# Performance work log

Measured on AMD Instinct MI355X. Metric: run time of the kernel, lower is better.

Reference implementation:

```python
import jax, jax.numpy as jnp
import numpy as np

WEIGHT = 1.0  # configer affinity_loss weight


def setup_inputs() -> dict:
    key = jax.random.key(0)
    k1, k2, k3, k4, k5 = jax.random.split(key, 5)
    bz, C, h, w = 4, 21, 32, 32
    token_n = h * w            # 1024
    total_n = token_n + 1      # 1025 (CLS token in encoder attns)
    head_n = 8
    return {
        "preds": jax.random.normal(k1, (bz, C, h, w), dtype=jnp.float32),
        "low_feats": jnp.zeros((1,), dtype=jnp.float32),
        "high_feats": jnp.zeros((1,), dtype=jnp.float32),
        "unlabeled_ROIs": jax.random.randint(k2, (bz, h, w), 0, 2, dtype=jnp.int32),
        "targets": jax.random.randint(k3, (bz, h, w), 0, C),
        # raw (pre-renormalization) positive attention maps, stacked over 2 layers
        "attns": jax.random.uniform(k4, (2, bz, head_n, total_n, total_n), dtype=jnp.float32),
        "decode_attns": jax.random.uniform(k5, (2, bz, head_n, token_n, token_n), dtype=jnp.float32),
    }


def reference(preds, low_feats, high_feats, unlabeled_ROIs, targets, attns, decode_attns):
    # loss_index=2, gt_add=0
    bz, C, h, w = preds.shape
    token_n = h * w
    Le = attns.shape[0]
    Ld = decode_attns.shape[0]

    # Encoder attentions: drop CLS row/col, row-normalize, average over heads & layers.
    enc = attns[:, :, :, 1:, 1:]                         # (Le, b, H, t, t)
    enc = enc / enc.sum(axis=-1, keepdims=True)
    encode_attn_avg = enc.mean(axis=(0, 2))              # (b, t, t)

    # Decoder attentions: crop to token_n, row-normalize, average over heads & layers.
    dec = decode_attns[:, :, :, :token_n, :token_n]
    dec = dec / dec.sum(axis=-1, keepdims=True)
    decode_attn_avg = dec.mean(axis=(0, 2))              # (b, t, t)

    total_attn_avg = (encode_attn_avg * Le + decode_attn_avg * Ld) / (Le + Ld)

    # Class probabilities per token: (b, t, C)
    prob = jax.nn.softmax(preds, axis=1).reshape(bz, C, token_n).transpose(0, 2, 1)

    # The broadcast-multiply-sum over dim=2 is exactly a batched matmul.
    affinity_prob = jnp.einsum('bij,bjc->bic', total_attn_avg, prob)
    affinity_prob = affinity_prob / affinity_prob.sum(axis=-1, keepdims=True)

    # nearest-interp to (h, w) is the identity here (ROIs already at (h, w))
    roi = unlabeled_ROIs.astype(jnp.float32).reshape(bz, token_n, 1)
    N = roi.sum()
    loss = (roi * jnp.abs(prob - affinity_prob)).sum()
    loss = jnp.where(N > 0, loss / N, loss)
    return WEIGHT * loss
```

## Files before the change

### kernel.cpp

```cpp
#include <hip/hip_runtime.h>
#include <cstdint>
#include <cstddef>

#define C_N     21
#define BZ      4
#define TOKEN_N 1024
#define TOTAL_N 1025
#define PROB_ELEMS (BZ * TOKEN_N * C_N)
#define ENC_TOT  67240000ull

typedef short  short8 __attribute__((ext_vector_type(8)));
typedef float  f32x4  __attribute__((ext_vector_type(4)));

typedef __attribute__((address_space(1))) const unsigned int* gld_gp;
typedef __attribute__((address_space(3))) unsigned int*       gld_lp;

static __device__ __forceinline__ unsigned int f2bf(float x) {
    unsigned int u = __float_as_uint(x);
    return (u + 0x7FFFu + ((u >> 16) & 1u)) >> 16;
}

__global__ __launch_bounds__(256) void softmax_kernel(const float* __restrict__ preds,
                                                      float* __restrict__ prob) {
    int t = blockIdx.x * blockDim.x + threadIdx.x;
    if (t >= BZ * TOKEN_N) return;
    int b = t >> 10, j = t & 1023;
    const float* p = preds + (size_t)b * C_N * TOKEN_N + j;
    float v[C_N];
    float mx = -3.4e38f;
#pragma unroll
    for (int c = 0; c < C_N; ++c) { v[c] = p[(size_t)c * TOKEN_N]; mx = fmaxf(mx, v[c]); }
    float ss = 0.f;
#pragma unroll
    for (int c = 0; c < C_N; ++c) { v[c] = __expf(v[c] - mx); ss += v[c]; }
    float inv = 1.f / ss;
    float* o = prob + (size_t)t * C_N;
#pragma unroll
    for (int c = 0; c < C_N; ++c) o[c] = v[c] * inv;
}

__global__ __launch_bounds__(256) void bpack2_kernel(const float* __restrict__ prob,
                                                     uint4* __restrict__ bp) {
    int idx = blockIdx.x * 256 + threadIdx.x;
    if (idx >= BZ * 32 * 2 * 64) return;
    int lane = idx & 63;
    int nt   = (idx >> 6) & 1;
    int kk   = (idx >> 7) & 31;
    int b    = idx >> 12;
    int n    = (lane & 15) + nt * 16;
    int k0   = kk * 32 + ((lane >> 4) << 3);
    unsigned int h[8];
#pragma unroll
    for (int e = 0; e < 8; ++e) {
        float v;
        if (n < C_N)       v = prob[((size_t)b * TOKEN_N + (k0 + e)) * C_N + n];
        else if (n == C_N) v = 1.0f;
        else               v = 0.0f;
        h[e] = f2bf(v);
    }
    uint4 o;
    o.x = h[0] | (h[1] << 16);
    o.y = h[2] | (h[3] << 16);
    o.z = h[4] | (h[5] << 16);
    o.w = h[6] | (h[7] << 16);
    bp[idx] = o;
}

template<bool ENC>
__device__ __forceinline__ void rows_body(const float* __restrict__ base, int mm, int i0,
                                          const uint4* __restrict__ bp,
                                          float* __restrict__ acc, float* __restrict__ lds) {
    const int tid  = threadIdx.x;
    const int lane = tid & 63;
    const int w    = tid >> 6;
    const int b    = (mm >> 3) & 3;

    int delta = 0;
    if constexpr (ENC) {
        const size_t S0 = (size_t)mm * 1050625ull + (size_t)(1 + i0) * 1025ull + 1ull;
        const size_t aligned = S0 & ~(size_t)3;
        delta = (int)(S0 - aligned);
        const int nInstr = (w < 3) ? 17 : 14;
        const int e0 = w * 17;
        for (int q = 0; q < nInstr; ++q) {
            const int e = e0 + q;
            size_t gb  = aligned + (size_t)e * 256;
            int   ldso = e * 256;
            if (gb + 256 > ENC_TOT) {
                size_t d = gb + 256 - ENC_TOT;
                gb -= d; ldso -= (int)d;
            }
            __builtin_amdgcn_global_load_lds((gld_gp)(base + gb + (size_t)lane * 4),
                                             (gld_lp)&lds[ldso], 16, 0, 0);
        }
    } else {
        const size_t sb = (size_t)mm * 1048576ull + (size_t)i0 * 1024ull;
#pragma unroll
        for (int q = 0; q < 16; ++q) {
            const int e = w * 16 + q;
            const int row = e >> 2, sub = e & 3;
            const size_t gb = sb + (size_t)row * 1024 + (size_t)sub * 256;
            const int ldso  = row * 1028 + sub * 256;
            __builtin_amdgcn_global_load_lds((gld_gp)(base + gb + (size_t)lane * 4),
                                             (gld_lp)&lds[ldso], 16, 0, 0);
        }
    }

    const uint4* bpp = bp + (size_t)b * 4096 + lane;
    uint4 Bq[8][2];
#pragma unroll
    for (int s = 0; s < 8; ++s) {
        Bq[s][0] = bpp[(w * 8 + s) * 128];
        Bq[s][1] = bpp[(w * 8 + s) * 128 + 64];
    }

    __syncthreads();

    const int r = lane & 15, kg = lane >> 4;
    f32x4 c0 = {0.f, 0.f, 0.f, 0.f};
    f32x4 c1 = {0.f, 0.f, 0.f, 0.f};
#pragma unroll
    for (int s = 0; s < 8; ++s) {
        const int k0 = w * 256 + s * 32 + kg * 8;
        float a0, a1, a2, a3, a4, a5, a6, a7;
        if constexpr (ENC) {
            const float* p = lds + delta + r * 1025 + k0;
            a0 = p[0]; a1 = p[1]; a2 = p[2]; a3 = p[3];
            a4 = p[4]; a5 = p[5]; a6 = p[6]; a7 = p[7];
        } else {
            const float* p = lds + r * 1028 + k0;
            float4 lo = *reinterpret_cast<const float4*>(p);
            float4 hi = *reinterpret_cast<const float4*>(p + 4);
            a0 = lo.x; a1 = lo.y; a2 = lo.z; a3 = lo.w;
            a4 = hi.x; a5 = hi.y; a6 = hi.z; a7 = hi.w;
        }
        uint4 aw;
        aw.x = f2bf(a0) | (f2bf(a1) << 16);
        aw.y = f2bf(a2) | (f2bf(a3) << 16);
        aw.z = f2bf(a4) | (f2bf(a5) << 16);
        aw.w = f2bf(a6) | (f2bf(a7) << 16);
        short8 af = __builtin_bit_cast(short8, aw);
        c0 = __builtin_amdgcn_mfma_f32_16x16x32_bf16(af, __builtin_bit_cast(short8, Bq[s][0]), c0, 0, 0, 0);
        c1 = __builtin_amdgcn_mfma_f32_16x16x32_bf16(af, __builtin_bit_cast(short8, Bq[s][1]), c1, 0, 0, 0);
    }

    __syncthreads();
    if (w != 0) {
        float* red = lds + w * 512 + lane * 8;
#pragma unroll
        for (int j = 0; j < 4; ++j) { red[j] = c0[j]; red[4 + j] = c1[j]; }
    }
    __syncthreads();
    if (w == 0) {
#pragma unroll
        for (int ww = 1; ww < 4; ++ww) {
            const float* red = lds + ww * 512 + lane * 8;
#pragma unroll
            for (int j = 0; j < 4; ++j) { c0[j] += red[j]; c1[j] += red[4 + j]; }
        }
#pragma unroll
        for (int rr = 0; rr < 4; ++rr) {
            float sv  = __shfl(c1[rr], (lane & 48) + 5);
            float inv = 1.0f / sv;
            int i = i0 + kg * 4 + rr;
            float* ao = acc + ((size_t)b * TOKEN_N + i) * C_N;
            unsafeAtomicAdd(&ao[r], c0[rr] * inv);
            if (r < C_N - 16) unsafeAtomicAdd(&ao[16 + r], c1[rr] * inv);
        }
    }
}

__global__ __launch_bounds__(256) void rows7_kernel(const float* __restrict__ attns,
                                                    const float* __restrict__ dattns,
                                                    const uint4* __restrict__ bp,
                                                    float* __restrict__ acc) {
    __shared__ __align__(16) float lds[16640];
    const int wid = blockIdx.x;
    const int m   = wid >> 6;
    const int i0  = (wid & 63) << 4;
    if (m < 64) rows_body<true >(attns,  m,      i0, bp, acc, lds);
    else        rows_body<false>(dattns, m - 64, i0, bp, acc, lds);
}

__global__ __launch_bounds__(256) void loss_kernel(const float* __restrict__ prob,
                                                   const float* __restrict__ acc,
                                                   const int* __restrict__ roi,
                                                   float* __restrict__ scal) {
    int t = blockIdx.x * 256 + threadIdx.x;
    float lossp = 0.f, np = 0.f;
    if (t < BZ * TOKEN_N) {
        int rv = roi[t];
        np = (float)rv;
        const float* a = acc + (size_t)t * C_N;
        const float* p = prob + (size_t)t * C_N;
        float S = 0.f;
#pragma unroll
        for (int c = 0; c < C_N; ++c) S += a[c];
        float invS = 1.f / S;
        float l = 0.f;
#pragma unroll
        for (int c = 0; c < C_N; ++c) l += fabsf(p[c] - a[c] * invS);
        lossp = rv ? l : 0.f;
    }
#pragma unroll
    for (int off = 32; off > 0; off >>= 1) {
        lossp += __shfl_down(lossp, off);
        np    += __shfl_down(np, off);
    }
    __shared__ float redL[4], redN[4];
    int lane = threadIdx.x & 63, wv = threadIdx.x >> 6;
    if (lane == 0) { redL[wv] = lossp; redN[wv] = np; }
    __syncthreads();
    if (threadIdx.x == 0) {
        float L  = redL[0] + redL[1] + redL[2] + redL[3];
        float NN = redN[0] + redN[1] + redN[2] + redN[3];
        unsafeAtomicAdd(&scal[0], L);
        unsafeAtomicAdd(&scal[1], NN);
    }
}

__global__ void finalize_kernel(const float* __restrict__ scal, float* __restrict__ out) {
    float loss = scal[0], N = scal[1];
    out[0] = (N > 0.f) ? (loss / N) : loss;
}

extern "C" void kernel_launch(void* const* d_in, const int* in_sizes, int n_in,
                              void* d_out, int out_size, void* d_ws, size_t ws_size,
                              hipStream_t stream) {
    const float* preds  = (const float*)d_in[0];
    const int*   roi    = (const int*)d_in[3];
    const float* attns  = (const float*)d_in[5];
    const float* dattns = (const float*)d_in[6];

    float* prob = (float*)d_ws;
    float* acc  = prob + PROB_ELEMS;
    float* scal = acc + PROB_ELEMS;
    uint4* bpack = (uint4*)((char*)d_ws + ((PROB_ELEMS * 2 + 2) * sizeof(float) + 15 & ~(size_t)15));

    hipMemsetAsync(acc, 0, (PROB_ELEMS + 2) * sizeof(float), stream);

    hipLaunchKernelGGL(softmax_kernel, dim3((BZ * TOKEN_N + 255) / 256), dim3(256), 0, stream,
                       preds, prob);
    hipLaunchKernelGGL(bpack2_kernel, dim3(64), dim3(256), 0, stream,
                       prob, bpack);
    hipLaunchKernelGGL(rows7_kernel, dim3(8192), dim3(256), 0, stream,
                       attns, dattns, bpack, acc);
    hipLaunchKernelGGL(loss_kernel, dim3((BZ * TOKEN_N + 255) / 256), dim3(256), 0, stream,
                       prob, acc, roi, scal);
    hipLaunchKernelGGL(finalize_kernel, dim3(1), dim3(1), 0, stream,
                       scal, (float*)d_out);
}
```

Before: 127.4 us.

## Fuse softmax with bf16 B-packing, fold finalize into loss, add streaming cache hint

Merges the softmax and bf16 B-operand packing kernels into one kernel that stages probabilities in shared memory. The finalize kernel is folded into the loss kernel through a last-block-done atomic counter. The attention loads into LDS now carry cache policy bit 2, likely a non-temporal or streaming hint for data read only once. Together these remove two launches and an extra round trip of prob through global memory. The cost is a small softmax grid with mostly idle threads and a counter reset that depends on the memset covering it.

```diff
diff --git a/kernel.cpp b/kernel.cpp
--- a/kernel.cpp
+++ b/kernel.cpp
@@ -20,50 +20,47 @@
     return (u + 0x7FFFu + ((u >> 16) & 1u)) >> 16;
 }
 
-__global__ __launch_bounds__(256) void softmax_kernel(const float* __restrict__ preds,
-                                                      float* __restrict__ prob) {
-    int t = blockIdx.x * blockDim.x + threadIdx.x;
-    if (t >= BZ * TOKEN_N) return;
-    int b = t >> 10, j = t & 1023;
-    const float* p = preds + (size_t)b * C_N * TOKEN_N + j;
-    float v[C_N];
-    float mx = -3.4e38f;
-#pragma unroll
-    for (int c = 0; c < C_N; ++c) { v[c] = p[(size_t)c * TOKEN_N]; mx = fmaxf(mx, v[c]); }
-    float ss = 0.f;
-#pragma unroll
-    for (int c = 0; c < C_N; ++c) { v[c] = __expf(v[c] - mx); ss += v[c]; }
-    float inv = 1.f / ss;
-    float* o = prob + (size_t)t * C_N;
-#pragma unroll
-    for (int c = 0; c < C_N; ++c) o[c] = v[c] * inv;
-}
-
-__global__ __launch_bounds__(256) void bpack2_kernel(const float* __restrict__ prob,
-                                                     uint4* __restrict__ bp) {
-    int idx = blockIdx.x * 256 + threadIdx.x;
-    if (idx >= BZ * 32 * 2 * 64) return;
-    int lane = idx & 63;
-    int nt   = (idx >> 6) & 1;
-    int kk   = (idx >> 7) & 31;
-    int b    = idx >> 12;
-    int n    = (lane & 15) + nt * 16;
-    int k0   = kk * 32 + ((lane >> 4) << 3);
+__global__ __launch_bounds__(128) void sb_kernel(const float* __restrict__ preds,
+                                                 float* __restrict__ prob,
+                                                 uint4* __restrict__ bp) {
+    const int b  = blockIdx.x >> 5;
+    const int kk = blockIdx.x & 31;
+    const int tid = threadIdx.x;
+    __shared__ float sm[32][33];
+
+    if (tid < 32) {
+        const int j = kk * 32 + tid;
+        const float* p = preds + (size_t)b * C_N * TOKEN_N + j;
+        float v[C_N];
+        float mx = -3.4e38f;
+#pragma unroll
+        for (int c = 0; c < C_N; ++c) { v[c] = p[(size_t)c * TOKEN_N]; mx = fmaxf(mx, v[c]); }
+        float ss = 0.f;
+#pragma unroll
+        for (int c = 0; c < C_N; ++c) { v[c] = __expf(v[c] - mx); ss += v[c]; }
+        float inv = 1.f / ss;
+        float* o = prob + ((size_t)b * TOKEN_N + j) * C_N;
+#pragma unroll
+        for (int c = 0; c < C_N; ++c) { float pv = v[c] * inv; o[c] = pv; sm[tid][c] = pv; }
+        sm[tid][C_N] = 1.0f;
+#pragma unroll
+        for (int c = C_N + 1; c < 32; ++c) sm[tid][c] = 0.f;
+    }
+    __syncthreads();
+
+    const int lane = tid & 63;
+    const int nt   = tid >> 6;
+    const int n    = (lane & 15) + nt * 16;
+    const int kl   = (lane >> 4) << 3;
     unsigned int h[8];
 #pragma unroll
-    for (int e = 0; e < 8; ++e) {
-        float v;
-        if (n < C_N)       v = prob[((size_t)b * TOKEN_N + (k0 + e)) * C_N + n];
-        else if (n == C_N) v = 1.0f;
-        else               v = 0.0f;
-        h[e] = f2bf(v);
-    }
+    for (int e = 0; e < 8; ++e) h[e] = f2bf(sm[kl + e][n]);
     uint4 o;
     o.x = h[0] | (h[1] << 16);
     o.y = h[2] | (h[3] << 16);
     o.z = h[4] | (h[5] << 16);
     o.w = h[6] | (h[7] << 16);
-    bp[idx] = o;
+    bp[(size_t)b * 4096 + kk * 128 + nt * 64 + lane] = o;
 }
 
 template<bool ENC>
@@ -91,7 +88,7 @@
                 gb -= d; ldso -= (int)d;
             }
             __builtin_amdgcn_global_load_lds((gld_gp)(base + gb + (size_t)lane * 4),
-                                             (gld_lp)&lds[ldso], 16, 0, 0);
+                                             (gld_lp)&lds[ldso], 16, 0, 2 );
         }
     } else {
         const size_t sb = (size_t)mm * 1048576ull + (size_t)i0 * 1024ull;
@@ -102,7 +99,7 @@
             const size_t gb = sb + (size_t)row * 1024 + (size_t)sub * 256;
             const int ldso  = row * 1028 + sub * 256;
             __builtin_amdgcn_global_load_lds((gld_gp)(base + gb + (size_t)lane * 4),
-                                             (gld_lp)&lds[ldso], 16, 0, 0);
+                                             (gld_lp)&lds[ldso], 16, 0, 2 );
         }
     }
 
@@ -170,7 +167,7 @@
     }
 }
 
-__global__ __launch_bounds__(256) void rows7_kernel(const float* __restrict__ attns,
+__global__ __launch_bounds__(256) void rows8_kernel(const float* __restrict__ attns,
                                                     const float* __restrict__ dattns,
                                                     const uint4* __restrict__ bp,
                                                     float* __restrict__ acc) {
@@ -182,10 +179,13 @@
     else        rows_body<false>(dattns, m - 64, i0, bp, acc, lds);
 }
 
-__global__ __launch_bounds__(256) void loss_kernel(const float* __restrict__ prob,
-                                                   const float* __restrict__ acc,
-                                                   const int* __restrict__ roi,
-                                                   float* __restrict__ scal) {
+__global__ __launch_bounds__(256) void loss2_kernel(const float* __restrict__ prob,
+                                                    const float* __restrict__ acc,
+                                                    const int* __restrict__ roi,
+                                                    float* __restrict__ scal,
+                                                    int* __restrict__ cnt,
+                                                    float* __restrict__ out,
+                                                    int nblocks) {
     int t = blockIdx.x * 256 + threadIdx.x;
     float lossp = 0.f, np = 0.f;
     if (t < BZ * TOKEN_N) {
@@ -216,12 +216,14 @@
         float NN = redN[0] + redN[1] + redN[2] + redN[3];
         unsafeAtomicAdd(&scal[0], L);
         unsafeAtomicAdd(&scal[1], NN);
-    }
-}
-
-__global__ void finalize_kernel(const float* __restrict__ scal, float* __restrict__ out) {
-    float loss = scal[0], N = scal[1];
-    out[0] = (N > 0.f) ? (loss / N) : loss;
+        __threadfence();
+        int prev = atomicAdd(cnt, 1);
+        if (prev == nblocks - 1) {
+            float loss = atomicAdd(&scal[0], 0.0f);
+            float N    = atomicAdd(&scal[1], 0.0f);
+            out[0] = (N > 0.f) ? (loss / N) : loss;
+        }
+    }
 }
 
 extern "C" void kernel_launch(void* const* d_in, const int* in_sizes, int n_in,
@@ -235,18 +237,16 @@
     float* prob = (float*)d_ws;
     float* acc  = prob + PROB_ELEMS;
     float* scal = acc + PROB_ELEMS;
-    uint4* bpack = (uint4*)((char*)d_ws + ((PROB_ELEMS * 2 + 2) * sizeof(float) + 15 & ~(size_t)15));
-
-    hipMemsetAsync(acc, 0, (PROB_ELEMS + 2) * sizeof(float), stream);
-
-    hipLaunchKernelGGL(softmax_kernel, dim3((BZ * TOKEN_N + 255) / 256), dim3(256), 0, stream,
-                       preds, prob);
-    hipLaunchKernelGGL(bpack2_kernel, dim3(64), dim3(256), 0, stream,
-                       prob, bpack);
-    hipLaunchKernelGGL(rows7_kernel, dim3(8192), dim3(256), 0, stream,
+    int*   cnt  = (int*)(scal + 2);
+    uint4* bpack = (uint4*)((char*)d_ws + ((PROB_ELEMS * 2 + 4) * sizeof(float) + 15 & ~(size_t)15));
+
+    hipMemsetAsync(acc, 0, (PROB_ELEMS + 3) * sizeof(float), stream);
+
+    hipLaunchKernelGGL(sb_kernel, dim3(BZ * 32), dim3(128), 0, stream,
+                       preds, prob, bpack);
+    hipLaunchKernelGGL(rows8_kernel, dim3(8192), dim3(256), 0, stream,
                        attns, dattns, bpack, acc);
-    hipLaunchKernelGGL(loss_kernel, dim3((BZ * TOKEN_N + 255) / 256), dim3(256), 0, stream,
-                       prob, acc, roi, scal);
-    hipLaunchKernelGGL(finalize_kernel, dim3(1), dim3(1), 0, stream,
-                       scal, (float*)d_out);
-}
+    const int LB = (BZ * TOKEN_N + 255) / 256;
+    hipLaunchKernelGGL(loss2_kernel, dim3(LB), dim3(256), 0, stream,
+                       prob, acc, roi, scal, cnt, (float*)d_out, LB);
+}
```

Result: faster. 120.1 us (-5.7%).
